# Optimization experiments

Measured on AMD Instinct MI355X. Metric: run time of the kernel, lower is better.

Reference implementation:

```python
import jax, jax.numpy as jnp
import numpy as np
import math

HIDDEN = 1024
HEADS = 16
HEAD = HIDDEN // HEADS  # 64
SCALE_BASE = 512.0


def _gammas(heads):
    # 1 - exp(linspace(log(1/32), log(1/512), heads))
    return 1.0 - jnp.exp(jnp.linspace(math.log(1.0 / 32.0), math.log(1.0 / 512.0), heads))


def _xpos(x, downscale):
    # x: [B, H, S, d]  (same head_size d for every head -> shared tables)
    S, d = x.shape[2], x.shape[3]
    half = d // 2
    base_scale = (jnp.arange(0, d, 2, dtype=jnp.float32) + 0.4 * d) / (1.4 * d)  # [half]
    pos = jnp.arange(S, dtype=jnp.float32)
    scale = base_scale[None, :] ** (pos / SCALE_BASE)[:, None]  # [S, half]
    if downscale:
        scale = 1.0 / scale
    inv_freq = 1.0 / (10000.0 ** (jnp.arange(half, dtype=jnp.float32) / half))
    sinusoid = pos[:, None] * inv_freq[None, :]  # [S, half]
    # duplicate-interleave (each column repeated twice)
    sin = jnp.repeat(jnp.sin(sinusoid) * scale, 2, axis=-1)  # [S, d]
    cos = jnp.repeat(jnp.cos(sinusoid) * scale, 2, axis=-1)  # [S, d]
    x1 = x[..., ::2]
    x2 = x[..., 1::2]
    rot = jnp.stack([-x2, x1], axis=-1).reshape(x.shape)  # rotate_every_two
    return x * cos + rot * sin


def _decay_mask(S, gammas):
    # D[h, n, m] = gamma_h^(n-m) for n >= m else 0
    n = jnp.arange(S)[:, None]
    m = jnp.arange(S)[None, :]
    diff = (n - m).astype(jnp.float32)
    mask = (n >= m)
    pw = jnp.maximum(diff, 0.0)[None, :, :]  # avoid overflow on negative diffs
    return jnp.where(mask[None, :, :], gammas[:, None, None] ** pw, 0.0)  # [H, S, S]


def retention_forward(Q, K, V):
    B, S, _ = Q.shape
    # split heads: [B, S, HIDDEN] -> [B, H, S, HEAD]
    def split(x, hd):
        return x.reshape(B, S, HEADS, hd).transpose(0, 2, 1, 3)
    q = _xpos(split(Q, HEAD), downscale=False)
    k = _xpos(split(K, HEAD), downscale=True)
    v = split(V, HEAD)
    D = _decay_mask(S, _gammas(HEADS).astype(Q.dtype))  # [H, S, S]
    scores = jnp.einsum('bhsd,bhtd->bhst', q, k) * D[None]
    out = jnp.einsum('bhst,bhtd->bhsd', scores, v)
    return out.transpose(0, 2, 1, 3).reshape(B, S, HEADS * HEAD)


def setup_inputs() -> dict:
    key = jax.random.key(0)
    kq, kk, kv = jax.random.split(key, 3)
    B, S = 2, 2048
    return {
        'Q': jax.random.normal(kq, (B, S, HIDDEN), dtype=jnp.float32),
        'K': jax.random.normal(kk, (B, S, HIDDEN), dtype=jnp.float32),
        'V': jax.random.normal(kv, (B, S, HIDDEN), dtype=jnp.float32),
    }


def reference(Q, K, V):
    return retention_forward(Q, K, V)
```

## Files before the change

### kernel.cpp

```cpp
#include <hip/hip_runtime.h>
#include <hip/hip_bf16.h>
#include <math.h>

#define B_  2
#define S_  2048
#define H_  16
#define D_  64

typedef __attribute__((ext_vector_type(8))) short bf16x8_t;
typedef __attribute__((ext_vector_type(4))) float f32x4_t;

__device__ __forceinline__ unsigned short f2bf(float f) {
    __hip_bfloat16 h = __float2bfloat16(f);
    return __builtin_bit_cast(unsigned short, h);
}
__device__ __forceinline__ float bf2f(unsigned short u) {
    unsigned int x = ((unsigned int)u) << 16;
    return __builtin_bit_cast(float, x);
}

__global__ __launch_bounds__(256) void prep1_kernel(const float* __restrict__ Q,
                                                    const float* __restrict__ K,
                                                    unsigned short* __restrict__ qb,
                                                    unsigned short* __restrict__ kb) {
    __shared__ float4 rotq[4 * 32];
    __shared__ float  gl[4 * 16 * 2];
    int t   = threadIdx.x;
    int bid = blockIdx.x;

    if (t < 128) {
        int sl = t >> 5, i = t & 31;
        int s  = (bid * 4 + sl) & 2047;
        float pos = (float)s;
        float bsc  = (2.0f * (float)i + 25.6f) / 89.6f;
        float xsc  = exp2f(log2f(bsc) * pos * (1.0f / 512.0f));
        float invf = exp2f(-(float)i * (13.287712379549449f / 32.0f));
        float ang  = pos * invf;
        float kq = rintf(ang * 0.15915494309189535f);
        float rr = fmaf(kq, -6.2831853071795865f, ang);
        float sn = sinf(rr), cs = cosf(rr);
        float rxs = 1.0f / xsc;
        rotq[sl * 32 + i] = make_float4(cs * xsc, sn * xsc, cs * rxs, sn * rxs);
    } else {
        int u  = t - 128;
        int sl = u >> 5, hh = (u >> 1) & 15, pm = u & 1;
        int s  = (bid * 4 + sl) & 2047;
        float lnv = -3.4657359027997265f + (float)hh * (-0.18483924814931874f);
        float l2g = log2f(1.0f - expf(lnv));
        gl[(sl * 16 + hh) * 2 + pm] = exp2f((pm ? -(float)s : (float)s) * l2g);
    }
    __syncthreads();

    int hh = t >> 4, i8 = t & 15;
#pragma unroll
    for (int j = 0; j < 4; ++j) {
        int r = bid * 4 + j;
        float4 r0 = rotq[j * 32 + 2 * i8];
        float4 r1 = rotq[j * 32 + 2 * i8 + 1];
        float gx = gl[(j * 16 + hh) * 2 + 0];
        float gy = gl[(j * 16 + hh) * 2 + 1];

        long idx = (long)r * 1024 + t * 4;
        float4 xq = *(const float4*)(Q + idx);
        float4 xk = *(const float4*)(K + idx);

        float cq0 = r0.x * gx, sq0 = r0.y * gx;
        float ck0 = r0.z * gy, sk0 = r0.w * gy;
        float cq1 = r1.x * gx, sq1 = r1.y * gx;
        float ck1 = r1.z * gy, sk1 = r1.w * gy;

        float q0 = xq.x * cq0 - xq.y * sq0, q1 = xq.y * cq0 + xq.x * sq0;
        float q2 = xq.z * cq1 - xq.w * sq1, q3 = xq.w * cq1 + xq.z * sq1;
        float k0 = xk.x * ck0 - xk.y * sk0, k1 = xk.y * ck0 + xk.x * sk0;
        float k2 = xk.z * ck1 - xk.w * sk1, k3 = xk.w * ck1 + xk.z * sk1;

        *(uint2*)(qb + idx) = make_uint2((unsigned)f2bf(q0) | ((unsigned)f2bf(q1) << 16),
                                         (unsigned)f2bf(q2) | ((unsigned)f2bf(q3) << 16));
        *(uint2*)(kb + idx) = make_uint2((unsigned)f2bf(k0) | ((unsigned)f2bf(k1) << 16),
                                         (unsigned)f2bf(k2) | ((unsigned)f2bf(k3) << 16));
    }
}

__global__ __launch_bounds__(256) void gchunkT_kernel(const float* __restrict__ V,
                                                      const unsigned short* __restrict__ kb,
                                                      unsigned short* __restrict__ vt,
                                                      unsigned short* __restrict__ Gg) {
    __shared__ float tileF[64 * 65];
    __shared__ __align__(16) unsigned short vtile[64 * 72];
    __shared__ __align__(16) unsigned short ktile[64 * 72];
    int t = threadIdx.x;
    int idx = blockIdx.x;
    int bh = idx >> 5, j = idx & 31;
    int b = bh >> 4, hh = bh & 15;
    int s0 = j * 64;
    int d = t >> 2, c = t & 3;

#pragma unroll
    for (int it = 0; it < 4; ++it) {
        int f  = it * 256 + t;
        int sl = f >> 4, d4 = f & 15;
        float4 v = *(const float4*)(V + ((long)(b * S_ + s0 + sl)) * 1024 + hh * 64 + d4 * 4);
        tileF[sl * 65 + d4 * 4 + 0] = v.x;
        tileF[sl * 65 + d4 * 4 + 1] = v.y;
        tileF[sl * 65 + d4 * 4 + 2] = v.z;
        tileF[sl * 65 + d4 * 4 + 3] = v.w;
    }
    __syncthreads();
    {
        unsigned int pk[8];
#pragma unroll
        for (int jj = 0; jj < 8; ++jj) {
            float f0 = tileF[(c * 16 + 2 * jj + 0) * 65 + d];
            float f1 = tileF[(c * 16 + 2 * jj + 1) * 65 + d];
            pk[jj] = (unsigned int)f2bf(f0) | ((unsigned int)f2bf(f1) << 16);
        }
        uint4 u0 = make_uint4(pk[0], pk[1], pk[2], pk[3]);
        uint4 u1 = make_uint4(pk[4], pk[5], pk[6], pk[7]);
        ((uint4*)&vtile[d * 72 + c * 16])[0] = u0;
        ((uint4*)&vtile[d * 72 + c * 16 + 8])[0] = u1;
        unsigned short* outp = vt + ((long)(bh * 64 + d)) * S_ + s0 + c * 16;
        ((uint4*)outp)[0] = u0;
        ((uint4*)outp)[1] = u1;
    }
    __syncthreads();
#pragma unroll
    for (int it = 0; it < 4; ++it) {
        int f  = it * 256 + t;
        int sl = f >> 4, d4 = f & 15;
        uint2 u = *(const uint2*)(kb + ((long)(b * S_ + s0 + sl)) * 1024 + hh * 64 + d4 * 4);
        tileF[sl * 65 + d4 * 4 + 0] = bf2f((unsigned short)(u.x & 0xffff));
        tileF[sl * 65 + d4 * 4 + 1] = bf2f((unsigned short)(u.x >> 16));
        tileF[sl * 65 + d4 * 4 + 2] = bf2f((unsigned short)(u.y & 0xffff));
        tileF[sl * 65 + d4 * 4 + 3] = bf2f((unsigned short)(u.y >> 16));
    }
    __syncthreads();
    {
        unsigned int pk[8];
#pragma unroll
        for (int jj = 0; jj < 8; ++jj) {
            float f0 = tileF[(c * 16 + 2 * jj + 0) * 65 + d];
            float f1 = tileF[(c * 16 + 2 * jj + 1) * 65 + d];
            pk[jj] = (unsigned int)f2bf(f0) | ((unsigned int)f2bf(f1) << 16);
        }
        ((uint4*)&ktile[d * 72 + c * 16])[0] = make_uint4(pk[0], pk[1], pk[2], pk[3]);
        ((uint4*)&ktile[d * 72 + c * 16 + 8])[0] = make_uint4(pk[4], pk[5], pk[6], pk[7]);
    }
    __syncthreads();

    int w = t >> 6, lane = t & 63, quad = lane >> 4, l16 = lane & 15;
    f32x4_t accS[4];
#pragma unroll
    for (int dkt = 0; dkt < 4; ++dkt) accS[dkt] = (f32x4_t){0.f, 0.f, 0.f, 0.f};

    bf16x8_t aV[2], bK[4][2];
#pragma unroll
    for (int sst = 0; sst < 2; ++sst)
        aV[sst] = *(const bf16x8_t*)&vtile[(w * 16 + l16) * 72 + sst * 32 + quad * 8];
#pragma unroll
    for (int dkt = 0; dkt < 4; ++dkt)
#pragma unroll
        for (int sst = 0; sst < 2; ++sst)
            bK[dkt][sst] = *(const bf16x8_t*)&ktile[(dkt * 16 + l16) * 72 + sst * 32 + quad * 8];
#pragma unroll
    for (int dkt = 0; dkt < 4; ++dkt)
#pragma unroll
        for (int sst = 0; sst < 2; ++sst)
            accS[dkt] = __builtin_amdgcn_mfma_f32_16x16x32_bf16(aV[sst], bK[dkt][sst], accS[dkt], 0, 0, 0);

    unsigned short* Gp = Gg + (long)idx * 4096;
#pragma unroll
    for (int dkt = 0; dkt < 4; ++dkt)
#pragma unroll
        for (int r = 0; r < 4; ++r)
            Gp[(w * 16 + quad * 4 + r) * 64 + dkt * 16 + l16] = f2bf(accS[dkt][r]);
}

__global__ __launch_bounds__(256) void scan_kernel(const unsigned short* __restrict__ Gg,
                                                   unsigned short* __restrict__ Sg) {
    int tid = blockIdx.x * 256 + threadIdx.x;
    int bh  = tid >> 12;
    int e   = tid & 4095;
    long base = ((long)bh * 32) * 4096 + e;
    float acc = 0.0f;
#pragma unroll
    for (int j = 0; j < 32; ++j) {
        if (j > 0) Sg[base + (long)j * 4096] = f2bf(acc);
        acc += bf2f(Gg[base + (long)j * 4096]);
    }
}

__global__ __launch_bounds__(256) void outc_kernel(const unsigned short* __restrict__ qb,
                                                   const unsigned short* __restrict__ kb,
                                                   const unsigned short* __restrict__ vt,
                                                   const unsigned short* __restrict__ Sg,
                                                   float* __restrict__ out) {
    __shared__ __align__(16) unsigned short strip[4][16 * 72];
    int t = threadIdx.x;
    int w = t >> 6, lane = t & 63, quad = lane >> 4, l16 = lane & 15;
    int idx = blockIdx.x;
    int bh  = idx & 31;
    int tch = idx >> 5;
    int b = bh >> 4, hh = bh & 15;

    const unsigned short* qB = qb + ((long)(b * S_ + tch * 64)) * 1024 + hh * 64;
    const unsigned short* kB = kb + ((long)(b * S_ + tch * 64)) * 1024 + hh * 64;
    const unsigned short* vB = vt + (long)bh * 64 * S_ + tch * 64;
    const unsigned short* SB = Sg + ((long)(bh * 32 + tch)) * 4096;

    bf16x8_t aQ[2];
#pragma unroll
    for (int kk = 0; kk < 2; ++kk)
        aQ[kk] = *(const bf16x8_t*)(qB + (long)(w * 16 + l16) * 1024 + kk * 32 + quad * 8);

    f32x4_t accO[4];
#pragma unroll
    for (int dvt = 0; dvt < 4; ++dvt) accO[dvt] = (f32x4_t){0.f, 0.f, 0.f, 0.f};

    if (tch > 0) {
#pragma unroll
        for (int dvt = 0; dvt < 4; ++dvt)
#pragma unroll
            for (int kk = 0; kk < 2; ++kk) {
                bf16x8_t bS = *(const bf16x8_t*)(SB + (dvt * 16 + l16) * 64 + kk * 32 + quad * 8);
                accO[dvt] = __builtin_amdgcn_mfma_f32_16x16x32_bf16(aQ[kk], bS, accO[dvt], 0, 0, 0);
            }
    }

    unsigned short* sw = strip[w];
    for (int st = w + 1; st < 4; ++st)
        *(uint2*)&sw[l16 * 72 + st * 16 + quad * 4] = make_uint2(0u, 0u);

    for (int st = 0; st <= w; ++st) {
        f32x4_t pp = (f32x4_t){0.f, 0.f, 0.f, 0.f};
#pragma unroll
        for (int kk = 0; kk < 2; ++kk) {
            bf16x8_t aK = *(const bf16x8_t*)(kB + (long)(st * 16 + l16) * 1024 + kk * 32 + quad * 8);
            pp = __builtin_amdgcn_mfma_f32_16x16x32_bf16(aK, aQ[kk], pp, 0, 0, 0);
        }
        if (st == w) {
#pragma unroll
            for (int r = 0; r < 4; ++r)
                if (quad * 4 + r > l16) pp[r] = 0.0f;
        }
        uint2 pk2;
        pk2.x = (unsigned)f2bf(pp[0]) | ((unsigned)f2bf(pp[1]) << 16);
        pk2.y = (unsigned)f2bf(pp[2]) | ((unsigned)f2bf(pp[3]) << 16);
        *(uint2*)&sw[l16 * 72 + st * 16 + quad * 4] = pk2;
    }

    bf16x8_t aP0 = *(const bf16x8_t*)&sw[l16 * 72 + 0 * 32 + quad * 8];
#pragma unroll
    for (int dvt = 0; dvt < 4; ++dvt) {
        bf16x8_t bV0 = *(const bf16x8_t*)(vB + (long)(dvt * 16 + l16) * S_ + 0 * 32 + quad * 8);
        accO[dvt] = __builtin_amdgcn_mfma_f32_16x16x32_bf16(aP0, bV0, accO[dvt], 0, 0, 0);
    }
    if (w >= 2) {
        bf16x8_t aP1 = *(const bf16x8_t*)&sw[l16 * 72 + 1 * 32 + quad * 8];
#pragma unroll
        for (int dvt = 0; dvt < 4; ++dvt) {
            bf16x8_t bV1 = *(const bf16x8_t*)(vB + (long)(dvt * 16 + l16) * S_ + 1 * 32 + quad * 8);
            accO[dvt] = __builtin_amdgcn_mfma_f32_16x16x32_bf16(aP1, bV1, accO[dvt], 0, 0, 0);
        }
    }

#pragma unroll
    for (int dvt = 0; dvt < 4; ++dvt)
#pragma unroll
        for (int r = 0; r < 4; ++r) {
            int row = tch * 64 + w * 16 + quad * 4 + r;
            out[((long)(b * S_ + row)) * 1024 + hh * 64 + dvt * 16 + l16] = accO[dvt][r];
        }
}

extern "C" void kernel_launch(void* const* d_in, const int* in_sizes, int n_in,
                              void* d_out, int out_size, void* d_ws, size_t ws_size,
                              hipStream_t stream) {
    const float* Q = (const float*)d_in[0];
    const float* K = (const float*)d_in[1];
    const float* V = (const float*)d_in[2];
    float* out = (float*)d_out;

    const size_t perBuf = (size_t)B_ * H_ * S_ * D_;
    unsigned short* qb = (unsigned short*)d_ws;
    unsigned short* kb = qb + perBuf;
    unsigned short* vt = kb + perBuf;
    unsigned short* Sg = vt + perBuf;
    unsigned short* Gg = Sg + perBuf;

    hipLaunchKernelGGL(prep1_kernel,   dim3(1024), dim3(256), 0, stream, Q, K, qb, kb);
    hipLaunchKernelGGL(gchunkT_kernel, dim3(1024), dim3(256), 0, stream, V, kb, vt, Gg);
    hipLaunchKernelGGL(scan_kernel,    dim3(512),  dim3(256), 0, stream, Gg, Sg);
    hipLaunchKernelGGL(outc_kernel,    dim3(1024), dim3(256), 0, stream, qb, kb, vt, Sg, out);
}
```

Before: 114.5 us.

## Fuse xPos rotation into chunk and output kernels, drop prep kernel

Removes the separate prep kernel that rotated and decay-scaled Q and K into bf16 buffers. K is now rotated inline in the chunk-state kernel, which writes kb itself, and Q is rotated on the fly in the output kernel straight from fp32 input. This saves one launch and the qb write/read round trip. In exchange, the sin/cos/exp work is recomputed per element instead of through shared per-row tables, and the output kernel now reads fp32 Q, twice the bytes of the old bf16 qb.

```diff
diff --git a/kernel.cpp b/kernel.cpp
--- a/kernel.cpp
+++ b/kernel.cpp
@@ -19,72 +19,23 @@
     return __builtin_bit_cast(float, x);
 }
 
-__global__ __launch_bounds__(256) void prep1_kernel(const float* __restrict__ Q,
-                                                    const float* __restrict__ K,
-                                                    unsigned short* __restrict__ qb,
-                                                    unsigned short* __restrict__ kb) {
-    __shared__ float4 rotq[4 * 32];
-    __shared__ float  gl[4 * 16 * 2];
-    int t   = threadIdx.x;
-    int bid = blockIdx.x;
-
-    if (t < 128) {
-        int sl = t >> 5, i = t & 31;
-        int s  = (bid * 4 + sl) & 2047;
-        float pos = (float)s;
-        float bsc  = (2.0f * (float)i + 25.6f) / 89.6f;
-        float xsc  = exp2f(log2f(bsc) * pos * (1.0f / 512.0f));
-        float invf = exp2f(-(float)i * (13.287712379549449f / 32.0f));
-        float ang  = pos * invf;
-        float kq = rintf(ang * 0.15915494309189535f);
-        float rr = fmaf(kq, -6.2831853071795865f, ang);
-        float sn = sinf(rr), cs = cosf(rr);
-        float rxs = 1.0f / xsc;
-        rotq[sl * 32 + i] = make_float4(cs * xsc, sn * xsc, cs * rxs, sn * rxs);
-    } else {
-        int u  = t - 128;
-        int sl = u >> 5, hh = (u >> 1) & 15, pm = u & 1;
-        int s  = (bid * 4 + sl) & 2047;
-        float lnv = -3.4657359027997265f + (float)hh * (-0.18483924814931874f);
-        float l2g = log2f(1.0f - expf(lnv));
-        gl[(sl * 16 + hh) * 2 + pm] = exp2f((pm ? -(float)s : (float)s) * l2g);
-    }
-    __syncthreads();
-
-    int hh = t >> 4, i8 = t & 15;
-#pragma unroll
-    for (int j = 0; j < 4; ++j) {
-        int r = bid * 4 + j;
-        float4 r0 = rotq[j * 32 + 2 * i8];
-        float4 r1 = rotq[j * 32 + 2 * i8 + 1];
-        float gx = gl[(j * 16 + hh) * 2 + 0];
-        float gy = gl[(j * 16 + hh) * 2 + 1];
-
-        long idx = (long)r * 1024 + t * 4;
-        float4 xq = *(const float4*)(Q + idx);
-        float4 xk = *(const float4*)(K + idx);
-
-        float cq0 = r0.x * gx, sq0 = r0.y * gx;
-        float ck0 = r0.z * gy, sk0 = r0.w * gy;
-        float cq1 = r1.x * gx, sq1 = r1.y * gx;
-        float ck1 = r1.z * gy, sk1 = r1.w * gy;
-
-        float q0 = xq.x * cq0 - xq.y * sq0, q1 = xq.y * cq0 + xq.x * sq0;
-        float q2 = xq.z * cq1 - xq.w * sq1, q3 = xq.w * cq1 + xq.z * sq1;
-        float k0 = xk.x * ck0 - xk.y * sk0, k1 = xk.y * ck0 + xk.x * sk0;
-        float k2 = xk.z * ck1 - xk.w * sk1, k3 = xk.w * ck1 + xk.z * sk1;
-
-        *(uint2*)(qb + idx) = make_uint2((unsigned)f2bf(q0) | ((unsigned)f2bf(q1) << 16),
-                                         (unsigned)f2bf(q2) | ((unsigned)f2bf(q3) << 16));
-        *(uint2*)(kb + idx) = make_uint2((unsigned)f2bf(k0) | ((unsigned)f2bf(k1) << 16),
-                                         (unsigned)f2bf(k2) | ((unsigned)f2bf(k3) << 16));
-    }
-}
-
-__global__ __launch_bounds__(256) void gchunkT_kernel(const float* __restrict__ V,
-                                                      const unsigned short* __restrict__ kb,
-                                                      unsigned short* __restrict__ vt,
-                                                      unsigned short* __restrict__ Gg) {
+__device__ __forceinline__ void rotpair(int i, float pos, float& cs_s, float& sn_s, bool down) {
+    float bsc  = (2.0f * (float)i + 25.6f) / 89.6f;
+    float xsc  = exp2f(log2f(bsc) * pos * (1.0f / 512.0f));
+    float invf = exp2f(-(float)i * (13.287712379549449f / 32.0f));
+    float ang  = pos * invf;
+    float kq = rintf(ang * 0.15915494309189535f);
+    float rr = fmaf(kq, -6.2831853071795865f, ang);
+    float sn = sinf(rr), cs = cosf(rr);
+    float sc = down ? (1.0f / xsc) : xsc;
+    cs_s = cs * sc; sn_s = sn * sc;
+}
+
+__global__ __launch_bounds__(256) void gkv_kernel(const float* __restrict__ K,
+                                                  const float* __restrict__ V,
+                                                  unsigned short* __restrict__ kb,
+                                                  unsigned short* __restrict__ vt,
+                                                  unsigned short* __restrict__ Gg) {
     __shared__ float tileF[64 * 65];
     __shared__ __align__(16) unsigned short vtile[64 * 72];
     __shared__ __align__(16) unsigned short ktile[64 * 72];
@@ -95,6 +46,9 @@
     int s0 = j * 64;
     int d = t >> 2, c = t & 3;
 
+    float lnv = -3.4657359027997265f + (float)hh * (-0.18483924814931874f);
+    float l2g = log2f(1.0f - expf(lnv));
+
 #pragma unroll
     for (int it = 0; it < 4; ++it) {
         int f  = it * 256 + t;
@@ -127,11 +81,23 @@
     for (int it = 0; it < 4; ++it) {
         int f  = it * 256 + t;
         int sl = f >> 4, d4 = f & 15;
-        uint2 u = *(const uint2*)(kb + ((long)(b * S_ + s0 + sl)) * 1024 + hh * 64 + d4 * 4);
-        tileF[sl * 65 + d4 * 4 + 0] = bf2f((unsigned short)(u.x & 0xffff));
-        tileF[sl * 65 + d4 * 4 + 1] = bf2f((unsigned short)(u.x >> 16));
-        tileF[sl * 65 + d4 * 4 + 2] = bf2f((unsigned short)(u.y & 0xffff));
-        tileF[sl * 65 + d4 * 4 + 3] = bf2f((unsigned short)(u.y >> 16));
+        float pos = (float)(s0 + sl);
+        long a = ((long)(b * S_ + s0 + sl)) * 1024 + hh * 64 + d4 * 4;
+        float4 xk = *(const float4*)(K + a);
+        float gsi = exp2f(-pos * l2g);
+        float c0, s0f, c1, s1f;
+        rotpair(2 * d4 + 0, pos, c0, s0f, true);
+        rotpair(2 * d4 + 1, pos, c1, s1f, true);
+        float ck0 = c0 * gsi, sk0 = s0f * gsi;
+        float ck1 = c1 * gsi, sk1 = s1f * gsi;
+        float k0 = xk.x * ck0 - xk.y * sk0, k1 = xk.y * ck0 + xk.x * sk0;
+        float k2 = xk.z * ck1 - xk.w * sk1, k3 = xk.w * ck1 + xk.z * sk1;
+        tileF[sl * 65 + d4 * 4 + 0] = k0;
+        tileF[sl * 65 + d4 * 4 + 1] = k1;
+        tileF[sl * 65 + d4 * 4 + 2] = k2;
+        tileF[sl * 65 + d4 * 4 + 3] = k3;
+        *(uint2*)(kb + a) = make_uint2((unsigned)f2bf(k0) | ((unsigned)f2bf(k1) << 16),
+                                       (unsigned)f2bf(k2) | ((unsigned)f2bf(k3) << 16));
     }
     __syncthreads();
     {
@@ -189,7 +155,7 @@
     }
 }
 
-__global__ __launch_bounds__(256) void outc_kernel(const unsigned short* __restrict__ qb,
+__global__ __launch_bounds__(256) void outc_kernel(const float* __restrict__ Q,
                                                    const unsigned short* __restrict__ kb,
                                                    const unsigned short* __restrict__ vt,
                                                    const unsigned short* __restrict__ Sg,
@@ -202,15 +168,38 @@
     int tch = idx >> 5;
     int b = bh >> 4, hh = bh & 15;
 
-    const unsigned short* qB = qb + ((long)(b * S_ + tch * 64)) * 1024 + hh * 64;
     const unsigned short* kB = kb + ((long)(b * S_ + tch * 64)) * 1024 + hh * 64;
     const unsigned short* vB = vt + (long)bh * 64 * S_ + tch * 64;
     const unsigned short* SB = Sg + ((long)(bh * 32 + tch)) * 4096;
 
+    float lnv = -3.4657359027997265f + (float)hh * (-0.18483924814931874f);
+    float l2g = log2f(1.0f - expf(lnv));
+    int qrow = w * 16 + l16;
+    float pos = (float)(tch * 64 + qrow);
+    float gs = exp2f(pos * l2g);
+    const float* Qp = Q + ((long)(b * S_ + tch * 64 + qrow)) * 1024 + hh * 64;
+
     bf16x8_t aQ[2];
 #pragma unroll
-    for (int kk = 0; kk < 2; ++kk)
-        aQ[kk] = *(const bf16x8_t*)(qB + (long)(w * 16 + l16) * 1024 + kk * 32 + quad * 8);
+    for (int kk = 0; kk < 2; ++kk) {
+        int d0 = kk * 32 + quad * 8;
+        float4 x0 = *(const float4*)(Qp + d0);
+        float4 x1 = *(const float4*)(Qp + d0 + 4);
+        float xs0 = x0.x, xs1 = x0.y, xs2 = x0.z, xs3 = x0.w;
+        float xs4 = x1.x, xs5 = x1.y, xs6 = x1.z, xs7 = x1.w;
+        bf16x8_t q;
+#pragma unroll
+        for (int p = 0; p < 4; ++p) {
+            float cv, sv;
+            rotpair(d0 / 2 + p, pos, cv, sv, false);
+            float cq = cv * gs, sq = sv * gs;
+            float xe = (p == 0) ? xs0 : (p == 1) ? xs2 : (p == 2) ? xs4 : xs6;
+            float xo = (p == 0) ? xs1 : (p == 1) ? xs3 : (p == 2) ? xs5 : xs7;
+            q[2 * p]     = (short)f2bf(xe * cq - xo * sq);
+            q[2 * p + 1] = (short)f2bf(xo * cq + xe * sq);
+        }
+        aQ[kk] = q;
+    }
 
     f32x4_t accO[4];
 #pragma unroll
@@ -281,14 +270,12 @@
     float* out = (float*)d_out;
 
     const size_t perBuf = (size_t)B_ * H_ * S_ * D_;
-    unsigned short* qb = (unsigned short*)d_ws;
-    unsigned short* kb = qb + perBuf;
+    unsigned short* kb = (unsigned short*)d_ws;
     unsigned short* vt = kb + perBuf;
     unsigned short* Sg = vt + perBuf;
     unsigned short* Gg = Sg + perBuf;
 
-    hipLaunchKernelGGL(prep1_kernel,   dim3(1024), dim3(256), 0, stream, Q, K, qb, kb);
-    hipLaunchKernelGGL(gchunkT_kernel, dim3(1024), dim3(256), 0, stream, V, kb, vt, Gg);
-    hipLaunchKernelGGL(scan_kernel,    dim3(512),  dim3(256), 0, stream, Gg, Sg);
-    hipLaunchKernelGGL(outc_kernel,    dim3(1024), dim3(256), 0, stream, qb, kb, vt, Sg, out);
-}
+    hipLaunchKernelGGL(gkv_kernel,  dim3(1024), dim3(256), 0, stream, K, V, kb, vt, Gg);
+    hipLaunchKernelGGL(scan_kernel, dim3(512),  dim3(256), 0, stream, Gg, Sg);
+    hipLaunchKernelGGL(outc_kernel, dim3(1024), dim3(256), 0, stream, Q, kb, vt, Sg, out);
+}
```

Result: faster. 111.2 us (-2.8%).
